# Performance work log

Hardware: AMD Instinct MI355X
Metric: run time of the kernel (lower is better)

## Reference

```python
import jax, jax.numpy as jnp
import numpy as np

N_NODES = 100000


def gcn_conv(x, src, dst, W, b, n):
    """PyG GCNConv: add self-loops, symmetric normalization, out = A_hat @ (x W) + b."""
    loop = jnp.arange(n, dtype=src.dtype)
    s = jnp.concatenate([src, loop])
    d = jnp.concatenate([dst, loop])
    deg = jnp.zeros((n,), dtype=x.dtype).at[d].add(1.0)
    dinv = jnp.where(deg > 0, jax.lax.rsqrt(deg), 0.0)
    norm = dinv[s] * dinv[d]                      # [E+N]
    h = x @ W                                     # [N, out]
    msg = h[s] * norm[:, None]                    # [E+N, out] gather
    out = jax.ops.segment_sum(msg, d, num_segments=n)  # scatter-add
    return out + b


def prelu(x, a):
    return jnp.where(x >= 0, x, a * x)


def setup_inputs() -> dict:
    key = jax.random.key(0)
    ks = jax.random.split(key, 12)
    n, din, dout, dproj = N_NODES, 128, 128, 128
    dhid = 2 * dout
    x = jax.random.normal(ks[0], (n, din), dtype=jnp.float32)
    edge_index = jax.random.randint(ks[1], (2, 1600000), 0, n, dtype=jnp.int64)

    def glorot(k, fan_in, fan_out):
        lim = np.sqrt(6.0 / (fan_in + fan_out))
        return jax.random.uniform(k, (fan_in, fan_out), jnp.float32, -lim, lim)

    return {
        "x": x,
        "edge_index": edge_index,
        "W1": glorot(ks[2], din, dhid),
        "b1": jnp.zeros((dhid,), jnp.float32),
        "W2": glorot(ks[3], dhid, dout),
        "b2": jnp.zeros((dout,), jnp.float32),
        "a": jnp.asarray(0.25, jnp.float32),          # PReLU weight (num_parameters=1)
        "fc1_w": glorot(ks[4], dout, dproj),
        "fc1_b": jnp.zeros((dproj,), jnp.float32),
        "fc2_w": glorot(ks[5], dproj, dout),
        "fc2_b": jnp.zeros((dout,), jnp.float32),
    }


def reference(x, edge_index, W1, b1, W2, b2, a, fc1_w, fc1_b, fc2_w, fc2_b):
    n = x.shape[0]
    src, dst = edge_index[0], edge_index[1]
    out = prelu(gcn_conv(x, src, dst, W1, b1, n), a)
    out = prelu(gcn_conv(out, src, dst, W2, b2, n), a)
    proj = jax.nn.relu(out @ fc1_w + fc1_b)
    proj = proj @ fc2_w + fc2_b
    return (out, proj)
```

## Files before the change

### kernel.cpp

```cpp
#include <hip/hip_runtime.h>


typedef __attribute__((ext_vector_type(4))) float  f32x4;
typedef __attribute__((ext_vector_type(8))) __bf16 bf16x8;
typedef __attribute__((ext_vector_type(8))) short  short8;

__device__ __forceinline__ bf16x8 as_bf(short8 s) {
    union { short8 s; bf16x8 b; } u; u.s = s; return u.b;
}

__device__ __forceinline__ short2 split1(float x) {
    unsigned u = __float_as_uint(x);
    short hi = (short)(u >> 16);
    float hif = __uint_as_float(u & 0xFFFF0000u);
    short lo = (short)(__float_as_uint(x - hif) >> 16);
    return make_short2(hi, lo);
}

__global__ void deg_kernel(const int* __restrict__ dst, int* __restrict__ deg, int E) {
    int e = blockIdx.x * blockDim.x + threadIdx.x;
    if (e < E) atomicAdd(&deg[dst[e]], 1);
}

__global__ __launch_bounds__(256)
void part_kernel(const int* __restrict__ deg, int* __restrict__ bsum,
                 float* __restrict__ dinv, int n) {
    int tid = threadIdx.x;
    int base = blockIdx.x * 1024 + tid * 4;
    int d[4] = {0, 0, 0, 0};
    if (base + 3 < n) {
        int4 v = *(const int4*)(deg + base);
        d[0] = v.x; d[1] = v.y; d[2] = v.z; d[3] = v.w;
    } else {
        for (int j = 0; j < 4; ++j) if (base + j < n) d[j] = deg[base + j];
    }
    for (int j = 0; j < 4; ++j)
        if (base + j < n) dinv[base + j] = rsqrtf((float)(d[j] + 1));
    int s = d[0] + d[1] + d[2] + d[3];
    for (int off = 32; off > 0; off >>= 1) s += __shfl_down(s, off);
    __shared__ int wsum[4];
    if ((tid & 63) == 0) wsum[tid >> 6] = s;
    __syncthreads();
    if (tid == 0) bsum[blockIdx.x] = wsum[0] + wsum[1] + wsum[2] + wsum[3];
}

__global__ __launch_bounds__(1024)
void topscan_kernel(const int* __restrict__ bsum, int* __restrict__ bbase, int nb) {
    __shared__ int sh[1024];
    int tid = threadIdx.x;
    int own = (tid < nb) ? bsum[tid] : 0;
    sh[tid] = own;
    __syncthreads();
    for (int off = 1; off < 1024; off <<= 1) {
        int t = (tid >= off) ? sh[tid - off] : 0;
        __syncthreads();
        sh[tid] += t;
        __syncthreads();
    }
    if (tid < nb) bbase[tid] = sh[tid] - own;
}

__global__ __launch_bounds__(256)
void offs_kernel(const int* __restrict__ deg, const int* __restrict__ bbase,
                 int* __restrict__ offsets, int n) {
    int tid = threadIdx.x;
    int base = blockIdx.x * 1024 + tid * 4;
    int d[4] = {0, 0, 0, 0};
    if (base + 3 < n) {
        int4 v = *(const int4*)(deg + base);
        d[0] = v.x; d[1] = v.y; d[2] = v.z; d[3] = v.w;
    } else {
        for (int j = 0; j < 4; ++j) if (base + j < n) d[j] = deg[base + j];
    }
    int s = d[0] + d[1] + d[2] + d[3];
    __shared__ int sh[256];
    sh[tid] = s;
    __syncthreads();
    for (int off = 1; off < 256; off <<= 1) {
        int t = (tid >= off) ? sh[tid - off] : 0;
        __syncthreads();
        sh[tid] += t;
        __syncthreads();
    }
    int run = bbase[blockIdx.x] + sh[tid] - s;
    for (int j = 0; j < 4; ++j) {
        int idx = base + j;
        if (idx <= n) offsets[idx] = run;
        if (idx < n) run += d[j];
    }
}

__global__ void fill_kernel(const int* __restrict__ src, const int* __restrict__ dst,
                            const int* __restrict__ offsets, int* __restrict__ cursor,
                            int* __restrict__ csr, int E) {
    int e = blockIdx.x * blockDim.x + threadIdx.x;
    if (e < E) {
        int d = dst[e];
        int pos = offsets[d] + atomicAdd(&cursor[d], 1);
        csr[pos] = src[e];
    }
}

__global__ void wconv_kernel(const float* __restrict__ W, short* __restrict__ Wt_hi,
                             short* __restrict__ Wt_lo, int K, int N) {
    int idx = blockIdx.x * blockDim.x + threadIdx.x;
    if (idx >= K * N) return;
    int nn = idx / K, kk = idx - nn * K;
    short2 s = split1(W[(size_t)kk * N + nn]);
    Wt_hi[idx] = s.x;
    Wt_lo[idx] = s.y;
}

__global__ __launch_bounds__(256)
void agg128_kernel(const float* __restrict__ g, const int* __restrict__ csr,
                   const int* __restrict__ offsets, const float* __restrict__ dinv,
                   const float* __restrict__ bias, const float* __restrict__ a_ptr,
                   float* __restrict__ out, int n) {
    int w = threadIdx.x >> 6;
    int lane = threadIdx.x & 63;
    int v = blockIdx.x * 4 + w;
    if (v >= n) return;
    const char* gb = (const char*)g;
    unsigned loff = (unsigned)lane * 8u;
    float dv = dinv[v];
    float2 self = *(const float2*)(gb + ((unsigned)v * 512u + loff));
    float accx = dv * self.x;
    float accy = dv * self.y;
    int e = offsets[v], end = offsets[v + 1];
#pragma unroll 1
    for (; e < end; e += 8) {
        int   idx[8];
        float dd[8];
        float2 mm[8];
#pragma unroll
        for (int j = 0; j < 8; ++j) {
            int ee = e + j;
            idx[j] = csr[ee < end ? ee : end - 1];
        }
#pragma unroll
        for (int j = 0; j < 8; ++j)
            dd[j] = (e + j < end) ? dinv[idx[j]] : 0.f;
#pragma unroll
        for (int j = 0; j < 8; ++j)
            mm[j] = *(const float2*)(gb + ((unsigned)idx[j] * 512u + loff));
#pragma unroll
        for (int j = 0; j < 8; ++j) {
            accx += dd[j] * mm[j].x;
            accy += dd[j] * mm[j].y;
        }
    }
    accx *= dv;
    accy *= dv;
    if (bias) {
        float a = *a_ptr;
        float2 bb = ((const float2*)bias)[lane];
        accx += bb.x;
        accy += bb.y;
        accx = accx >= 0.f ? accx : a * accx;
        accy = accy >= 0.f ? accy : a * accy;
    }
    float2 r; r.x = accx; r.y = accy;
    ((float2*)out)[(size_t)v * 64 + lane] = r;
}

__global__ __launch_bounds__(256)
void gemm64_kernel(const float* __restrict__ A, int lda,
                   const short* __restrict__ Bt_hi, const short* __restrict__ Bt_lo,
                   float* __restrict__ C, int M, int N, int k_base,
                   int mtiles, int tpb,
                   const float* __restrict__ bias, int act,
                   const float* __restrict__ a_ptr, int accum) {
    const int tid  = threadIdx.x;
    const int wave = tid >> 6, lane = tid & 63;
    const int quad = lane >> 4, l16 = lane & 15;
    const int col0 = blockIdx.y * 64;

    bf16x8 bf[4][4][2];
#pragma unroll
    for (int kt = 0; kt < 4; ++kt)
#pragma unroll
        for (int t = 0; t < 4; ++t) {
            size_t off = (size_t)(col0 + t * 16 + l16) * lda + k_base + kt * 32 + quad * 8;
            bf[kt][t][0] = as_bf(*(const short8*)(Bt_hi + off));
            bf[kt][t][1] = as_bf(*(const short8*)(Bt_lo + off));
        }

    const float aw = (act == 2) ? *a_ptr : 0.f;

    const int t0 = blockIdx.x * tpb;
    const int t1 = (t0 + tpb < mtiles) ? t0 + tpb : mtiles;
    for (int tile = t0; tile < t1; ++tile) {
        const int m = tile * 64 + wave * 16 + l16;
        const int mc = m < M ? m : M - 1;
        const float* Ap = A + (size_t)mc * lda + k_base + quad * 8;

        float4 av[8];
#pragma unroll
        for (int kt = 0; kt < 4; ++kt) {
            av[2 * kt]     = *(const float4*)(Ap + kt * 32);
            av[2 * kt + 1] = *(const float4*)(Ap + kt * 32 + 4);
        }

        f32x4 acc[4];
#pragma unroll
        for (int t = 0; t < 4; ++t) acc[t] = (f32x4){0.f, 0.f, 0.f, 0.f};

#pragma unroll
        for (int kt = 0; kt < 4; ++kt) {
            float4 v0 = av[2 * kt], v1 = av[2 * kt + 1];
            short8 ah, al;
            short2 s;
            s = split1(v0.x); ah[0] = s.x; al[0] = s.y;
            s = split1(v0.y); ah[1] = s.x; al[1] = s.y;
            s = split1(v0.z); ah[2] = s.x; al[2] = s.y;
            s = split1(v0.w); ah[3] = s.x; al[3] = s.y;
            s = split1(v1.x); ah[4] = s.x; al[4] = s.y;
            s = split1(v1.y); ah[5] = s.x; al[5] = s.y;
            s = split1(v1.z); ah[6] = s.x; al[6] = s.y;
            s = split1(v1.w); ah[7] = s.x; al[7] = s.y;
            bf16x8 a_hi = as_bf(ah), a_lo = as_bf(al);
#pragma unroll
            for (int t = 0; t < 4; ++t) {
                acc[t] = __builtin_amdgcn_mfma_f32_16x16x32_bf16(bf[kt][t][0], a_hi, acc[t], 0, 0, 0);
                acc[t] = __builtin_amdgcn_mfma_f32_16x16x32_bf16(bf[kt][t][1], a_hi, acc[t], 0, 0, 0);
                acc[t] = __builtin_amdgcn_mfma_f32_16x16x32_bf16(bf[kt][t][0], a_lo, acc[t], 0, 0, 0);
            }
        }

        if (m < M) {
            float* Crow = C + (size_t)m * N + col0 + quad * 4;
#pragma unroll
            for (int t = 0; t < 4; ++t) {
                float4 v;
                v.x = acc[t][0]; v.y = acc[t][1]; v.z = acc[t][2]; v.w = acc[t][3];
                if (accum) {
                    float4 o = *(const float4*)(Crow + t * 16);
                    v.x += o.x; v.y += o.y; v.z += o.z; v.w += o.w;
                }
                if (bias) {
                    float4 bb = *(const float4*)(bias + col0 + t * 16 + quad * 4);
                    v.x += bb.x; v.y += bb.y; v.z += bb.z; v.w += bb.w;
                }
                if (act == 1) {
                    v.x = fmaxf(v.x, 0.f); v.y = fmaxf(v.y, 0.f);
                    v.z = fmaxf(v.z, 0.f); v.w = fmaxf(v.w, 0.f);
                } else if (act == 2) {
                    v.x = v.x >= 0.f ? v.x : aw * v.x;
                    v.y = v.y >= 0.f ? v.y : aw * v.y;
                    v.z = v.z >= 0.f ? v.z : aw * v.z;
                    v.w = v.w >= 0.f ? v.w : aw * v.w;
                }
                *(float4*)(Crow + t * 16) = v;
            }
        }
    }
}

extern "C" void kernel_launch(void* const* d_in, const int* in_sizes, int n_in,
                              void* d_out, int out_size, void* d_ws, size_t ws_size,
                              hipStream_t stream) {
    const float* x     = (const float*)d_in[0];
    const int*   ei    = (const int*)d_in[1];
    const float* W1    = (const float*)d_in[2];
    const float* b1    = (const float*)d_in[3];
    const float* W2    = (const float*)d_in[4];
    const float* b2    = (const float*)d_in[5];
    const float* a_ptr = (const float*)d_in[6];
    const float* fc1_w = (const float*)d_in[7];
    const float* fc1_b = (const float*)d_in[8];
    const float* fc2_w = (const float*)d_in[9];
    const float* fc2_b = (const float*)d_in[10];

    const int n = in_sizes[0] / 128;
    const int E = in_sizes[1] / 2;
    const int* src = ei;
    const int* dst = ei + E;
    const int nb = (n + 1023) >> 10;

    float* out_final  = (float*)d_out;
    float* proj_final = out_final + (size_t)n * 128;
    float* out1       = (float*)d_out;

    char* p = (char*)d_ws;
    auto take = [&](size_t bytes) -> char* {
        char* q = p;
        p += (bytes + 1023) & ~(size_t)1023;
        return q;
    };
    int*   deg     = (int*)take((size_t)n * 4);
    int*   offsets = (int*)take(((size_t)n + 1) * 4);
    int*   cursor  = (int*)take((size_t)n * 4);
    float* dinv    = (float*)take((size_t)n * 4);
    int*   bsum    = (int*)take((size_t)1024 * 4);
    int*   bbase   = (int*)take((size_t)1024 * 4);
    int*   csr     = (int*)take((size_t)E * 4);
    short* W1t_hi  = (short*)take((size_t)256 * 128 * 2);
    short* W1t_lo  = (short*)take((size_t)256 * 128 * 2);
    short* W2t_hi  = (short*)take((size_t)128 * 256 * 2);
    short* W2t_lo  = (short*)take((size_t)128 * 256 * 2);
    short* f1t_hi  = (short*)take((size_t)128 * 128 * 2);
    short* f1t_lo  = (short*)take((size_t)128 * 128 * 2);
    short* f2t_hi  = (short*)take((size_t)128 * 128 * 2);
    short* f2t_lo  = (short*)take((size_t)128 * 128 * 2);
    float* bufA    = (float*)take((size_t)n * 128 * 4);

    (void)hipMemsetAsync(deg, 0, (size_t)n * 4, stream);
    (void)hipMemsetAsync(cursor, 0, (size_t)n * 4, stream);

    wconv_kernel<<<(128 * 256 + 255) / 256, 256, 0, stream>>>(W1, W1t_hi, W1t_lo, 128, 256);
    wconv_kernel<<<(256 * 128 + 255) / 256, 256, 0, stream>>>(W2, W2t_hi, W2t_lo, 256, 128);
    wconv_kernel<<<(128 * 128 + 255) / 256, 256, 0, stream>>>(fc1_w, f1t_hi, f1t_lo, 128, 128);
    wconv_kernel<<<(128 * 128 + 255) / 256, 256, 0, stream>>>(fc2_w, f2t_hi, f2t_lo, 128, 128);

    deg_kernel<<<(E + 255) / 256, 256, 0, stream>>>(dst, deg, E);
    part_kernel<<<nb, 256, 0, stream>>>(deg, bsum, dinv, n);
    topscan_kernel<<<1, 1024, 0, stream>>>(bsum, bbase, nb);
    offs_kernel<<<nb, 256, 0, stream>>>(deg, bbase, offsets, n);
    fill_kernel<<<(E + 255) / 256, 256, 0, stream>>>(src, dst, offsets, cursor, csr, E);

    const int mtiles = (n + 63) / 64;
    const int TPB = 4;
    const int gx = (mtiles + TPB - 1) / TPB;

    agg128_kernel<<<(n + 3) / 4, 256, 0, stream>>>(x, csr, offsets, dinv,
                                                   nullptr, nullptr, bufA, n);
    gemm64_kernel<<<dim3(gx, 4), 256, 0, stream>>>(bufA, 128, W1t_hi, W1t_lo, out1,
                                                   n, 256, 0, mtiles, TPB, b1, 2, a_ptr, 0);

    gemm64_kernel<<<dim3(gx, 2), 256, 0, stream>>>(out1, 256, W2t_hi, W2t_lo, bufA,
                                                   n, 128, 0, mtiles, TPB, nullptr, 0, nullptr, 0);
    gemm64_kernel<<<dim3(gx, 2), 256, 0, stream>>>(out1, 256, W2t_hi, W2t_lo, bufA,
                                                   n, 128, 128, mtiles, TPB, nullptr, 0, nullptr, 1);
    agg128_kernel<<<(n + 3) / 4, 256, 0, stream>>>(bufA, csr, offsets, dinv,
                                                   b2, a_ptr, out_final, n);

    gemm64_kernel<<<dim3(gx, 2), 256, 0, stream>>>(out_final, 128, f1t_hi, f1t_lo, bufA,
                                                   n, 128, 0, mtiles, TPB, fc1_b, 1, nullptr, 0);
    gemm64_kernel<<<dim3(gx, 2), 256, 0, stream>>>(bufA, 128, f2t_hi, f2t_lo, proj_final,
                                                   n, 128, 0, mtiles, TPB, fc2_b, 0, nullptr, 0);
}
```

Measured before the change: 816.2 us.

## Fuse consecutive GEMM pairs through LDS and widen aggregation unroll

Replaces the separate gemm64 launches with a templated fused2_kernel. It computes two back-to-back GEMMs per 16-row block, keeping the bias-and-activation intermediate as split bf16 hi/lo in swizzled shared memory. This removes the global write and re-read of the 256-wide hidden layer and the fc1 output, plus several launches. In exchange, every 16-row block reloads both weight matrices into registers, which raises L2 weight traffic and register pressure. Separately, the neighbour-gather loop in the aggregation kernel now unrolls 12 instead of 8 to keep more loads in flight.

```diff
diff --git a/kernel.cpp b/kernel.cpp
--- a/kernel.cpp
+++ b/kernel.cpp
@@ -15,6 +15,10 @@
     float hif = __uint_as_float(u & 0xFFFF0000u);
     short lo = (short)(__float_as_uint(x - hif) >> 16);
     return make_short2(hi, lo);
+}
+
+__device__ __forceinline__ unsigned pack2(short a, short b) {
+    return ((unsigned)(unsigned short)a) | ((unsigned)(unsigned short)b << 16);
 }
 
 __global__ void deg_kernel(const int* __restrict__ dst, int* __restrict__ deg, int E) {
@@ -128,23 +132,23 @@
     float accy = dv * self.y;
     int e = offsets[v], end = offsets[v + 1];
 #pragma unroll 1
-    for (; e < end; e += 8) {
-        int   idx[8];
-        float dd[8];
-        float2 mm[8];
-#pragma unroll
-        for (int j = 0; j < 8; ++j) {
+    for (; e < end; e += 12) {
+        int   idx[12];
+        float dd[12];
+        float2 mm[12];
+#pragma unroll
+        for (int j = 0; j < 12; ++j) {
             int ee = e + j;
             idx[j] = csr[ee < end ? ee : end - 1];
         }
 #pragma unroll
-        for (int j = 0; j < 8; ++j)
+        for (int j = 0; j < 12; ++j)
             dd[j] = (e + j < end) ? dinv[idx[j]] : 0.f;
 #pragma unroll
-        for (int j = 0; j < 8; ++j)
+        for (int j = 0; j < 12; ++j)
             mm[j] = *(const float2*)(gb + ((unsigned)idx[j] * 512u + loff));
 #pragma unroll
-        for (int j = 0; j < 8; ++j) {
+        for (int j = 0; j < 12; ++j) {
             accx += dd[j] * mm[j].x;
             accy += dd[j] * mm[j].y;
         }
@@ -163,95 +167,130 @@
     ((float2*)out)[(size_t)v * 64 + lane] = r;
 }
 
+template<int K1, int N1, int N2>
 __global__ __launch_bounds__(256)
-void gemm64_kernel(const float* __restrict__ A, int lda,
-                   const short* __restrict__ Bt_hi, const short* __restrict__ Bt_lo,
-                   float* __restrict__ C, int M, int N, int k_base,
-                   int mtiles, int tpb,
-                   const float* __restrict__ bias, int act,
-                   const float* __restrict__ a_ptr, int accum) {
+void fused2_kernel(const float* __restrict__ A,
+                   const short* __restrict__ B1h, const short* __restrict__ B1l,
+                   const short* __restrict__ B2h, const short* __restrict__ B2l,
+                   float* __restrict__ C, int M,
+                   const float* __restrict__ midbias,
+                   const float* __restrict__ mid_a,
+                   const float* __restrict__ bias2) {
+    constexpr int KT1 = K1 / 32;
+    constexpr int T1  = N1 / 64;
+    constexpr int KT2 = N1 / 32;
+    constexpr int T2  = N2 / 64;
+    __shared__ short hs[16 * N1];
+    __shared__ short ls[16 * N1];
+
     const int tid  = threadIdx.x;
-    const int wave = tid >> 6, lane = tid & 63;
+    const int w    = tid >> 6, lane = tid & 63;
     const int quad = lane >> 4, l16 = lane & 15;
-    const int col0 = blockIdx.y * 64;
-
-    bf16x8 bf[4][4][2];
-#pragma unroll
-    for (int kt = 0; kt < 4; ++kt)
-#pragma unroll
-        for (int t = 0; t < 4; ++t) {
-            size_t off = (size_t)(col0 + t * 16 + l16) * lda + k_base + kt * 32 + quad * 8;
-            bf[kt][t][0] = as_bf(*(const short8*)(Bt_hi + off));
-            bf[kt][t][1] = as_bf(*(const short8*)(Bt_lo + off));
-        }
-
-    const float aw = (act == 2) ? *a_ptr : 0.f;
-
-    const int t0 = blockIdx.x * tpb;
-    const int t1 = (t0 + tpb < mtiles) ? t0 + tpb : mtiles;
-    for (int tile = t0; tile < t1; ++tile) {
-        const int m = tile * 64 + wave * 16 + l16;
-        const int mc = m < M ? m : M - 1;
-        const float* Ap = A + (size_t)mc * lda + k_base + quad * 8;
-
-        float4 av[8];
-#pragma unroll
-        for (int kt = 0; kt < 4; ++kt) {
-            av[2 * kt]     = *(const float4*)(Ap + kt * 32);
-            av[2 * kt + 1] = *(const float4*)(Ap + kt * 32 + 4);
-        }
-
-        f32x4 acc[4];
-#pragma unroll
-        for (int t = 0; t < 4; ++t) acc[t] = (f32x4){0.f, 0.f, 0.f, 0.f};
-
-#pragma unroll
-        for (int kt = 0; kt < 4; ++kt) {
-            float4 v0 = av[2 * kt], v1 = av[2 * kt + 1];
-            short8 ah, al;
-            short2 s;
-            s = split1(v0.x); ah[0] = s.x; al[0] = s.y;
-            s = split1(v0.y); ah[1] = s.x; al[1] = s.y;
-            s = split1(v0.z); ah[2] = s.x; al[2] = s.y;
-            s = split1(v0.w); ah[3] = s.x; al[3] = s.y;
-            s = split1(v1.x); ah[4] = s.x; al[4] = s.y;
-            s = split1(v1.y); ah[5] = s.x; al[5] = s.y;
-            s = split1(v1.z); ah[6] = s.x; al[6] = s.y;
-            s = split1(v1.w); ah[7] = s.x; al[7] = s.y;
-            bf16x8 a_hi = as_bf(ah), a_lo = as_bf(al);
-#pragma unroll
-            for (int t = 0; t < 4; ++t) {
-                acc[t] = __builtin_amdgcn_mfma_f32_16x16x32_bf16(bf[kt][t][0], a_hi, acc[t], 0, 0, 0);
-                acc[t] = __builtin_amdgcn_mfma_f32_16x16x32_bf16(bf[kt][t][1], a_hi, acc[t], 0, 0, 0);
-                acc[t] = __builtin_amdgcn_mfma_f32_16x16x32_bf16(bf[kt][t][0], a_lo, acc[t], 0, 0, 0);
+    const int colb1 = w * (N1 / 4);
+    const int colb2 = w * (N2 / 4);
+    const unsigned sw = (unsigned)(l16 & 7) << 4;
+
+    const int m  = blockIdx.x * 16 + l16;
+    const int mc = m < M ? m : blockIdx.x * 16;
+
+    bf16x8 bf[T1][KT1][2];
+#pragma unroll
+    for (int t = 0; t < T1; ++t)
+#pragma unroll
+        for (int kt = 0; kt < KT1; ++kt) {
+            size_t off = (size_t)(colb1 + t * 16 + l16) * K1 + kt * 32 + quad * 8;
+            bf[t][kt][0] = as_bf(*(const short8*)(B1h + off));
+            bf[t][kt][1] = as_bf(*(const short8*)(B1l + off));
+        }
+    const float* Ap = A + (size_t)mc * K1 + quad * 8;
+    float4 av[KT1 * 2];
+#pragma unroll
+    for (int kt = 0; kt < KT1; ++kt) {
+        av[2 * kt]     = *(const float4*)(Ap + kt * 32);
+        av[2 * kt + 1] = *(const float4*)(Ap + kt * 32 + 4);
+    }
+    f32x4 acc[T1];
+#pragma unroll
+    for (int t = 0; t < T1; ++t) acc[t] = (f32x4){0.f, 0.f, 0.f, 0.f};
+
+#pragma unroll
+    for (int kt = 0; kt < KT1; ++kt) {
+        float4 v0 = av[2 * kt], v1 = av[2 * kt + 1];
+        short8 ah, al;
+        short2 s;
+        s = split1(v0.x); ah[0] = s.x; al[0] = s.y;
+        s = split1(v0.y); ah[1] = s.x; al[1] = s.y;
+        s = split1(v0.z); ah[2] = s.x; al[2] = s.y;
+        s = split1(v0.w); ah[3] = s.x; al[3] = s.y;
+        s = split1(v1.x); ah[4] = s.x; al[4] = s.y;
+        s = split1(v1.y); ah[5] = s.x; al[5] = s.y;
+        s = split1(v1.z); ah[6] = s.x; al[6] = s.y;
+        s = split1(v1.w); ah[7] = s.x; al[7] = s.y;
+        bf16x8 a_hi = as_bf(ah), a_lo = as_bf(al);
+#pragma unroll
+        for (int t = 0; t < T1; ++t) {
+            acc[t] = __builtin_amdgcn_mfma_f32_16x16x32_bf16(bf[t][kt][0], a_hi, acc[t], 0, 0, 0);
+            acc[t] = __builtin_amdgcn_mfma_f32_16x16x32_bf16(bf[t][kt][1], a_hi, acc[t], 0, 0, 0);
+            acc[t] = __builtin_amdgcn_mfma_f32_16x16x32_bf16(bf[t][kt][0], a_lo, acc[t], 0, 0, 0);
+        }
+    }
+
+    const float am = mid_a ? *mid_a : 0.f;
+#pragma unroll
+    for (int t = 0; t < T1; ++t) {
+        const int col = colb1 + t * 16 + quad * 4;
+        const float4 bb = *(const float4*)(midbias + col);
+        float v0 = acc[t][0] + bb.x; v0 = v0 >= 0.f ? v0 : am * v0;
+        float v1 = acc[t][1] + bb.y; v1 = v1 >= 0.f ? v1 : am * v1;
+        float v2 = acc[t][2] + bb.z; v2 = v2 >= 0.f ? v2 : am * v2;
+        float v3 = acc[t][3] + bb.w; v3 = v3 >= 0.f ? v3 : am * v3;
+        short2 s0 = split1(v0), s1 = split1(v1), s2 = split1(v2), s3 = split1(v3);
+        uint2 hp, lp;
+        hp.x = pack2(s0.x, s1.x); hp.y = pack2(s2.x, s3.x);
+        lp.x = pack2(s0.y, s1.y); lp.y = pack2(s2.y, s3.y);
+        const unsigned off = ((unsigned)(l16 * N1 + col) * 2u) ^ sw;
+        *(uint2*)((char*)hs + off) = hp;
+        *(uint2*)((char*)ls + off) = lp;
+    }
+    __syncthreads();
+
+    bf16x8 b2[T2][KT2][2];
+#pragma unroll
+    for (int t = 0; t < T2; ++t)
+#pragma unroll
+        for (int kt = 0; kt < KT2; ++kt) {
+            size_t off = (size_t)(colb2 + t * 16 + l16) * N1 + kt * 32 + quad * 8;
+            b2[t][kt][0] = as_bf(*(const short8*)(B2h + off));
+            b2[t][kt][1] = as_bf(*(const short8*)(B2l + off));
+        }
+    f32x4 acc2[T2];
+#pragma unroll
+    for (int t = 0; t < T2; ++t) acc2[t] = (f32x4){0.f, 0.f, 0.f, 0.f};
+
+#pragma unroll
+    for (int kt = 0; kt < KT2; ++kt) {
+        const unsigned off = ((unsigned)(l16 * N1 + kt * 32 + quad * 8) * 2u) ^ sw;
+        bf16x8 a_hi = *(const bf16x8*)((const char*)hs + off);
+        bf16x8 a_lo = *(const bf16x8*)((const char*)ls + off);
+#pragma unroll
+        for (int t = 0; t < T2; ++t) {
+            acc2[t] = __builtin_amdgcn_mfma_f32_16x16x32_bf16(b2[t][kt][0], a_hi, acc2[t], 0, 0, 0);
+            acc2[t] = __builtin_amdgcn_mfma_f32_16x16x32_bf16(b2[t][kt][1], a_hi, acc2[t], 0, 0, 0);
+            acc2[t] = __builtin_amdgcn_mfma_f32_16x16x32_bf16(b2[t][kt][0], a_lo, acc2[t], 0, 0, 0);
+        }
+    }
+
+    if (m < M) {
+        float* Crow = C + (size_t)m * N2 + colb2 + quad * 4;
+#pragma unroll
+        for (int t = 0; t < T2; ++t) {
+            float4 v;
+            v.x = acc2[t][0]; v.y = acc2[t][1]; v.z = acc2[t][2]; v.w = acc2[t][3];
+            if (bias2) {
+                const float4 bb = *(const float4*)(bias2 + colb2 + t * 16 + quad * 4);
+                v.x += bb.x; v.y += bb.y; v.z += bb.z; v.w += bb.w;
             }
-        }
-
-        if (m < M) {
-            float* Crow = C + (size_t)m * N + col0 + quad * 4;
-#pragma unroll
-            for (int t = 0; t < 4; ++t) {
-                float4 v;
-                v.x = acc[t][0]; v.y = acc[t][1]; v.z = acc[t][2]; v.w = acc[t][3];
-                if (accum) {
-                    float4 o = *(const float4*)(Crow + t * 16);
-                    v.x += o.x; v.y += o.y; v.z += o.z; v.w += o.w;
-                }
-                if (bias) {
-                    float4 bb = *(const float4*)(bias + col0 + t * 16 + quad * 4);
-                    v.x += bb.x; v.y += bb.y; v.z += bb.z; v.w += bb.w;
-                }
-                if (act == 1) {
-                    v.x = fmaxf(v.x, 0.f); v.y = fmaxf(v.y, 0.f);
-                    v.z = fmaxf(v.z, 0.f); v.w = fmaxf(v.w, 0.f);
-                } else if (act == 2) {
-                    v.x = v.x >= 0.f ? v.x : aw * v.x;
-                    v.y = v.y >= 0.f ? v.y : aw * v.y;
-                    v.z = v.z >= 0.f ? v.z : aw * v.z;
-                    v.w = v.w >= 0.f ? v.w : aw * v.w;
-                }
-                *(float4*)(Crow + t * 16) = v;
-            }
+            *(float4*)(Crow + t * 16) = v;
         }
     }
 }
@@ -279,7 +318,6 @@
 
     float* out_final  = (float*)d_out;
     float* proj_final = out_final + (size_t)n * 128;
-    float* out1       = (float*)d_out;
 
     char* p = (char*)d_ws;
     auto take = [&](size_t bytes) -> char* {
@@ -318,24 +356,16 @@
     offs_kernel<<<nb, 256, 0, stream>>>(deg, bbase, offsets, n);
     fill_kernel<<<(E + 255) / 256, 256, 0, stream>>>(src, dst, offsets, cursor, csr, E);
 
-    const int mtiles = (n + 63) / 64;
-    const int TPB = 4;
-    const int gx = (mtiles + TPB - 1) / TPB;
+    const int sblk = (n + 15) / 16;
 
     agg128_kernel<<<(n + 3) / 4, 256, 0, stream>>>(x, csr, offsets, dinv,
                                                    nullptr, nullptr, bufA, n);
-    gemm64_kernel<<<dim3(gx, 4), 256, 0, stream>>>(bufA, 128, W1t_hi, W1t_lo, out1,
-                                                   n, 256, 0, mtiles, TPB, b1, 2, a_ptr, 0);
-
-    gemm64_kernel<<<dim3(gx, 2), 256, 0, stream>>>(out1, 256, W2t_hi, W2t_lo, bufA,
-                                                   n, 128, 0, mtiles, TPB, nullptr, 0, nullptr, 0);
-    gemm64_kernel<<<dim3(gx, 2), 256, 0, stream>>>(out1, 256, W2t_hi, W2t_lo, bufA,
-                                                   n, 128, 128, mtiles, TPB, nullptr, 0, nullptr, 1);
+    fused2_kernel<128, 256, 128><<<sblk, 256, 0, stream>>>(
+        bufA, W1t_hi, W1t_lo, W2t_hi, W2t_lo, bufA, n, b1, a_ptr, nullptr);
+
     agg128_kernel<<<(n + 3) / 4, 256, 0, stream>>>(bufA, csr, offsets, dinv,
                                                    b2, a_ptr, out_final, n);
 
-    gemm64_kernel<<<dim3(gx, 2), 256, 0, stream>>>(out_final, 128, f1t_hi, f1t_lo, bufA,
-                                                   n, 128, 0, mtiles, TPB, fc1_b, 1, nullptr, 0);
-    gemm64_kernel<<<dim3(gx, 2), 256, 0, stream>>>(bufA, 128, f2t_hi, f2t_lo, proj_final,
-                                                   n, 128, 0, mtiles, TPB, fc2_b, 0, nullptr, 0);
-}
+    fused2_kernel<128, 128, 128><<<sblk, 256, 0, stream>>>(
+        out_final, f1t_hi, f1t_lo, f2t_hi, f2t_lo, proj_final, n, fc1_b, nullptr, fc2_b);
+}
```

Result: slower. 879.2 us (+7.7%).

## Fuse K-split W2 GEMM into one pass with fragment-packed weights

Applied to the files above, without the earlier changes.

Weights are now converted into an MFMA-fragment-ordered hi/lo bf16 layout so each lane loads its B fragment with one contiguous short8 read. The GEMM is templated on K-tiles and N-tiles, which lets the 256-deep W2 product run as a single kernel (32-wide column blocks, full K) instead of two launches with a read-modify-write accumulate. The aggregation gather loop is also unrolled from 8 to 12 neighbours to keep more loads in flight. In exchange there are more registers per thread for the B fragments and gathers, and the A rows of the W2 GEMM are reloaded by four column blocks instead of two.

```diff
diff --git a/kernel.cpp b/kernel.cpp
--- a/kernel.cpp
+++ b/kernel.cpp
@@ -101,14 +101,21 @@
     }
 }
 
-__global__ void wconv_kernel(const float* __restrict__ W, short* __restrict__ Wt_hi,
-                             short* __restrict__ Wt_lo, int K, int N) {
-    int idx = blockIdx.x * blockDim.x + threadIdx.x;
-    if (idx >= K * N) return;
-    int nn = idx / K, kk = idx - nn * K;
+__global__ void wconv_kernel(const float* __restrict__ W, short* __restrict__ Fh,
+                             short* __restrict__ Fl, int K, int N, int ktlog) {
+    int o = blockIdx.x * blockDim.x + threadIdx.x;
+    if (o >= K * N) return;
+    int j  = o & 7;
+    int l  = (o >> 3) & 15;
+    int q  = (o >> 7) & 3;
+    int t2 = o >> 9;
+    int kt = t2 & ((1 << ktlog) - 1);
+    int nt = t2 >> ktlog;
+    int nn = nt * 16 + l;
+    int kk = kt * 32 + q * 8 + j;
     short2 s = split1(W[(size_t)kk * N + nn]);
-    Wt_hi[idx] = s.x;
-    Wt_lo[idx] = s.y;
+    Fh[o] = s.x;
+    Fl[o] = s.y;
 }
 
 __global__ __launch_bounds__(256)
@@ -128,23 +135,23 @@
     float accy = dv * self.y;
     int e = offsets[v], end = offsets[v + 1];
 #pragma unroll 1
-    for (; e < end; e += 8) {
-        int   idx[8];
-        float dd[8];
-        float2 mm[8];
-#pragma unroll
-        for (int j = 0; j < 8; ++j) {
+    for (; e < end; e += 12) {
+        int   idx[12];
+        float dd[12];
+        float2 mm[12];
+#pragma unroll
+        for (int j = 0; j < 12; ++j) {
             int ee = e + j;
             idx[j] = csr[ee < end ? ee : end - 1];
         }
 #pragma unroll
-        for (int j = 0; j < 8; ++j)
+        for (int j = 0; j < 12; ++j)
             dd[j] = (e + j < end) ? dinv[idx[j]] : 0.f;
 #pragma unroll
-        for (int j = 0; j < 8; ++j)
+        for (int j = 0; j < 12; ++j)
             mm[j] = *(const float2*)(gb + ((unsigned)idx[j] * 512u + loff));
 #pragma unroll
-        for (int j = 0; j < 8; ++j) {
+        for (int j = 0; j < 12; ++j) {
             accx += dd[j] * mm[j].x;
             accy += dd[j] * mm[j].y;
         }
@@ -163,26 +170,28 @@
     ((float2*)out)[(size_t)v * 64 + lane] = r;
 }
 
+template<int KT, int T>
 __global__ __launch_bounds__(256)
 void gemm64_kernel(const float* __restrict__ A, int lda,
-                   const short* __restrict__ Bt_hi, const short* __restrict__ Bt_lo,
-                   float* __restrict__ C, int M, int N, int k_base,
+                   const short* __restrict__ Bh, const short* __restrict__ Bl,
+                   float* __restrict__ C, int M, int N,
                    int mtiles, int tpb,
                    const float* __restrict__ bias, int act,
-                   const float* __restrict__ a_ptr, int accum) {
+                   const float* __restrict__ a_ptr) {
     const int tid  = threadIdx.x;
     const int wave = tid >> 6, lane = tid & 63;
     const int quad = lane >> 4, l16 = lane & 15;
-    const int col0 = blockIdx.y * 64;
-
-    bf16x8 bf[4][4][2];
-#pragma unroll
-    for (int kt = 0; kt < 4; ++kt)
-#pragma unroll
-        for (int t = 0; t < 4; ++t) {
-            size_t off = (size_t)(col0 + t * 16 + l16) * lda + k_base + kt * 32 + quad * 8;
-            bf[kt][t][0] = as_bf(*(const short8*)(Bt_hi + off));
-            bf[kt][t][1] = as_bf(*(const short8*)(Bt_lo + off));
+    const int col0 = blockIdx.y * (T * 16);
+    const int nt0  = col0 >> 4;
+
+    bf16x8 bf[T][KT][2];
+#pragma unroll
+    for (int t = 0; t < T; ++t)
+#pragma unroll
+        for (int kt = 0; kt < KT; ++kt) {
+            size_t off = ((size_t)((nt0 + t) * KT + kt) << 9) + (lane << 3);
+            bf[t][kt][0] = as_bf(*(const short8*)(Bh + off));
+            bf[t][kt][1] = as_bf(*(const short8*)(Bl + off));
         }
 
     const float aw = (act == 2) ? *a_ptr : 0.f;
@@ -190,55 +199,54 @@
     const int t0 = blockIdx.x * tpb;
     const int t1 = (t0 + tpb < mtiles) ? t0 + tpb : mtiles;
     for (int tile = t0; tile < t1; ++tile) {
-        const int m = tile * 64 + wave * 16 + l16;
+        const int m  = tile * 64 + wave * 16 + l16;
         const int mc = m < M ? m : M - 1;
-        const float* Ap = A + (size_t)mc * lda + k_base + quad * 8;
-
-        float4 av[8];
-#pragma unroll
-        for (int kt = 0; kt < 4; ++kt) {
-            av[2 * kt]     = *(const float4*)(Ap + kt * 32);
-            av[2 * kt + 1] = *(const float4*)(Ap + kt * 32 + 4);
-        }
-
-        f32x4 acc[4];
-#pragma unroll
-        for (int t = 0; t < 4; ++t) acc[t] = (f32x4){0.f, 0.f, 0.f, 0.f};
-
-#pragma unroll
-        for (int kt = 0; kt < 4; ++kt) {
-            float4 v0 = av[2 * kt], v1 = av[2 * kt + 1];
-            short8 ah, al;
-            short2 s;
-            s = split1(v0.x); ah[0] = s.x; al[0] = s.y;
-            s = split1(v0.y); ah[1] = s.x; al[1] = s.y;
-            s = split1(v0.z); ah[2] = s.x; al[2] = s.y;
-            s = split1(v0.w); ah[3] = s.x; al[3] = s.y;
-            s = split1(v1.x); ah[4] = s.x; al[4] = s.y;
-            s = split1(v1.y); ah[5] = s.x; al[5] = s.y;
-            s = split1(v1.z); ah[6] = s.x; al[6] = s.y;
-            s = split1(v1.w); ah[7] = s.x; al[7] = s.y;
-            bf16x8 a_hi = as_bf(ah), a_lo = as_bf(al);
-#pragma unroll
-            for (int t = 0; t < 4; ++t) {
-                acc[t] = __builtin_amdgcn_mfma_f32_16x16x32_bf16(bf[kt][t][0], a_hi, acc[t], 0, 0, 0);
-                acc[t] = __builtin_amdgcn_mfma_f32_16x16x32_bf16(bf[kt][t][1], a_hi, acc[t], 0, 0, 0);
-                acc[t] = __builtin_amdgcn_mfma_f32_16x16x32_bf16(bf[kt][t][0], a_lo, acc[t], 0, 0, 0);
+        const float* Ap = A + (size_t)mc * lda + quad * 8;
+
+        f32x4 acc[T];
+#pragma unroll
+        for (int t = 0; t < T; ++t) acc[t] = (f32x4){0.f, 0.f, 0.f, 0.f};
+
+#pragma unroll
+        for (int kh = 0; kh < KT / 4; ++kh) {
+            float4 av[8];
+#pragma unroll
+            for (int kk = 0; kk < 4; ++kk) {
+                av[2 * kk]     = *(const float4*)(Ap + (kh * 4 + kk) * 32);
+                av[2 * kk + 1] = *(const float4*)(Ap + (kh * 4 + kk) * 32 + 4);
+            }
+#pragma unroll
+            for (int kk = 0; kk < 4; ++kk) {
+                const int kt = kh * 4 + kk;
+                float4 v0 = av[2 * kk], v1 = av[2 * kk + 1];
+                short8 ah, al;
+                short2 s;
+                s = split1(v0.x); ah[0] = s.x; al[0] = s.y;
+                s = split1(v0.y); ah[1] = s.x; al[1] = s.y;
+                s = split1(v0.z); ah[2] = s.x; al[2] = s.y;
+                s = split1(v0.w); ah[3] = s.x; al[3] = s.y;
+                s = split1(v1.x); ah[4] = s.x; al[4] = s.y;
+                s = split1(v1.y); ah[5] = s.x; al[5] = s.y;
+                s = split1(v1.z); ah[6] = s.x; al[6] = s.y;
+                s = split1(v1.w); ah[7] = s.x; al[7] = s.y;
+                bf16x8 a_hi = as_bf(ah), a_lo = as_bf(al);
+#pragma unroll
+                for (int t = 0; t < T; ++t) {
+                    acc[t] = __builtin_amdgcn_mfma_f32_16x16x32_bf16(bf[t][kt][0], a_hi, acc[t], 0, 0, 0);
+                    acc[t] = __builtin_amdgcn_mfma_f32_16x16x32_bf16(bf[t][kt][1], a_hi, acc[t], 0, 0, 0);
+                    acc[t] = __builtin_amdgcn_mfma_f32_16x16x32_bf16(bf[t][kt][0], a_lo, acc[t], 0, 0, 0);
+                }
             }
         }
 
         if (m < M) {
             float* Crow = C + (size_t)m * N + col0 + quad * 4;
 #pragma unroll
-            for (int t = 0; t < 4; ++t) {
+            for (int t = 0; t < T; ++t) {
                 float4 v;
                 v.x = acc[t][0]; v.y = acc[t][1]; v.z = acc[t][2]; v.w = acc[t][3];
-                if (accum) {
-                    float4 o = *(const float4*)(Crow + t * 16);
-                    v.x += o.x; v.y += o.y; v.z += o.z; v.w += o.w;
-                }
                 if (bias) {
-                    float4 bb = *(const float4*)(bias + col0 + t * 16 + quad * 4);
+                    const float4 bb = *(const float4*)(bias + col0 + t * 16 + quad * 4);
                     v.x += bb.x; v.y += bb.y; v.z += bb.z; v.w += bb.w;
                 }
                 if (act == 1) {
@@ -307,10 +315,10 @@
     (void)hipMemsetAsync(deg, 0, (size_t)n * 4, stream);
     (void)hipMemsetAsync(cursor, 0, (size_t)n * 4, stream);
 
-    wconv_kernel<<<(128 * 256 + 255) / 256, 256, 0, stream>>>(W1, W1t_hi, W1t_lo, 128, 256);
-    wconv_kernel<<<(256 * 128 + 255) / 256, 256, 0, stream>>>(W2, W2t_hi, W2t_lo, 256, 128);
-    wconv_kernel<<<(128 * 128 + 255) / 256, 256, 0, stream>>>(fc1_w, f1t_hi, f1t_lo, 128, 128);
-    wconv_kernel<<<(128 * 128 + 255) / 256, 256, 0, stream>>>(fc2_w, f2t_hi, f2t_lo, 128, 128);
+    wconv_kernel<<<(128 * 256 + 255) / 256, 256, 0, stream>>>(W1, W1t_hi, W1t_lo, 128, 256, 2);
+    wconv_kernel<<<(256 * 128 + 255) / 256, 256, 0, stream>>>(W2, W2t_hi, W2t_lo, 256, 128, 3);
+    wconv_kernel<<<(128 * 128 + 255) / 256, 256, 0, stream>>>(fc1_w, f1t_hi, f1t_lo, 128, 128, 2);
+    wconv_kernel<<<(128 * 128 + 255) / 256, 256, 0, stream>>>(fc2_w, f2t_hi, f2t_lo, 128, 128, 2);
 
     deg_kernel<<<(E + 255) / 256, 256, 0, stream>>>(dst, deg, E);
     part_kernel<<<nb, 256, 0, stream>>>(deg, bsum, dinv, n);
@@ -324,18 +332,16 @@
 
     agg128_kernel<<<(n + 3) / 4, 256, 0, stream>>>(x, csr, offsets, dinv,
                                                    nullptr, nullptr, bufA, n);
-    gemm64_kernel<<<dim3(gx, 4), 256, 0, stream>>>(bufA, 128, W1t_hi, W1t_lo, out1,
-                                                   n, 256, 0, mtiles, TPB, b1, 2, a_ptr, 0);
-
-    gemm64_kernel<<<dim3(gx, 2), 256, 0, stream>>>(out1, 256, W2t_hi, W2t_lo, bufA,
-                                                   n, 128, 0, mtiles, TPB, nullptr, 0, nullptr, 0);
-    gemm64_kernel<<<dim3(gx, 2), 256, 0, stream>>>(out1, 256, W2t_hi, W2t_lo, bufA,
-                                                   n, 128, 128, mtiles, TPB, nullptr, 0, nullptr, 1);
+    gemm64_kernel<4, 4><<<dim3(gx, 4), 256, 0, stream>>>(
+        bufA, 128, W1t_hi, W1t_lo, out1, n, 256, mtiles, TPB, b1, 2, a_ptr);
+
+    gemm64_kernel<8, 2><<<dim3(gx, 4), 256, 0, stream>>>(
+        out1, 256, W2t_hi, W2t_lo, bufA, n, 128, mtiles, TPB, nullptr, 0, nullptr);
     agg128_kernel<<<(n + 3) / 4, 256, 0, stream>>>(bufA, csr, offsets, dinv,
                                                    b2, a_ptr, out_final, n);
 
-    gemm64_kernel<<<dim3(gx, 2), 256, 0, stream>>>(out_final, 128, f1t_hi, f1t_lo, bufA,
-                                                   n, 128, 0, mtiles, TPB, fc1_b, 1, nullptr, 0);
-    gemm64_kernel<<<dim3(gx, 2), 256, 0, stream>>>(bufA, 128, f2t_hi, f2t_lo, proj_final,
-                                                   n, 128, 0, mtiles, TPB, fc2_b, 0, nullptr, 0);
-}
+    gemm64_kernel<4, 4><<<dim3(gx, 2), 256, 0, stream>>>(
+        out_final, 128, f1t_hi, f1t_lo, bufA, n, 128, mtiles, TPB, fc1_b, 1, nullptr);
+    gemm64_kernel<4, 4><<<dim3(gx, 2), 256, 0, stream>>>(
+        bufA, 128, f2t_hi, f2t_lo, proj_final, n, 128, mtiles, TPB, fc2_b, 0, nullptr);
+}
```

New measurement: 778.2 us. 1.05x faster.
